# Performance work log

Hardware: AMD Instinct MI355X
Metric: run time of the kernel (lower is better)

## Reference

```python
import jax, jax.numpy as jnp
import numpy as np

EPS = 1e-5
NUM_GN_GROUPS = 32


def setup_inputs() -> dict:
    key = jax.random.key(0)
    k1, k2, k3 = jax.random.split(key, 3)
    B, C, N, G = 2, 256, 4096, 8
    c = C // G
    return {
        "points": jax.random.normal(k1, (B, C, N), dtype=jnp.float32),
        "conv_w": jax.random.normal(k2, (G, c, c), dtype=jnp.float32) / np.sqrt(c),
        "conv_b": jax.random.normal(k3, (C,), dtype=jnp.float32) * 0.02,
        "gn_w": jnp.ones((C,), dtype=jnp.float32),
        "gn_b": jnp.zeros((C,), dtype=jnp.float32),
    }


def reference(points, conv_w, conv_b, gn_w, gn_b):
    B, C, N = points.shape
    G = conv_w.shape[0]
    c = C // G  # channels per attention group
    identity = points

    # grouped 1x1 conv: per-group [c,c] matmul + bias
    x = points.reshape(B, G, c, N)
    x = jnp.einsum('gij,bgjn->bgin', conv_w, x) + conv_b.reshape(1, G, c, 1)

    # attention[b,g,n,m] = sum_i x[b,g,i,n] * x[b,g,i,m] / sqrt(c)
    scale = 1.0 / np.sqrt(c).astype(np.float32)
    attn = jnp.einsum('bgin,bgim->bgnm', x, x) * scale
    # softmax over dim=2 (the query/row N axis -- non-standard)
    attn = jax.nn.softmax(attn, axis=2)

    # ELU-gated second matmul: [B,G,c,N] @ [B,G,N,N] -> [B,G,c,N]
    x = jnp.einsum('bgcn,bgnm->bgcm', jax.nn.elu(x), attn)

    # channel shuffle: [B,G,c,N] -> [B,c,G,N] -> [B,C,N]
    x = x.transpose(0, 2, 1, 3).reshape(B, C, N)
    x = x + identity

    # GroupNorm(32 groups) over (channels-in-group, N)
    xg = x.reshape(B, NUM_GN_GROUPS, C // NUM_GN_GROUPS, N)
    mean = xg.mean(axis=(2, 3), keepdims=True)
    var = xg.var(axis=(2, 3), keepdims=True)
    xg = (xg - mean) * jax.lax.rsqrt(var + EPS)
    x = xg.reshape(B, C, N)
    return x * gn_w.reshape(1, C, 1) + gn_b.reshape(1, C, 1)
```

## Files before the change

### kernel.cpp

```cpp
#include <hip/hip_runtime.h>

typedef __attribute__((ext_vector_type(8))) short bf16x8;
typedef __attribute__((ext_vector_type(4))) short bf16x4;
typedef __attribute__((ext_vector_type(4))) float f32x4;

#if __has_builtin(__builtin_amdgcn_exp2f)
#define EXP2(x) __builtin_amdgcn_exp2f(x)
#else
#define EXP2(x) exp2f(x)
#endif

__device__ __forceinline__ unsigned short f2bf(float f) {
    union { float f; unsigned int u; } v; v.f = f;
    unsigned int r = v.u + 0x7fffu + ((v.u >> 16) & 1u);
    return (unsigned short)(r >> 16);
}

__device__ __forceinline__ float asf(unsigned int u) {
    union { unsigned int u; float f; } v; v.u = u; return v.f;
}

#define QK_PRESCALE 0.50500983f

__global__ __launch_bounds__(256) void conv_kernel(
    const float* __restrict__ points, const float* __restrict__ conv_w,
    const float* __restrict__ conv_b,
    unsigned short* __restrict__ xqT, unsigned short* __restrict__ xv)
{
    __shared__ float w[1024];
    const int h  = blockIdx.x >> 4;
    const int nc = blockIdx.x & 15;
    const int g  = h & 7;
    const int tid = threadIdx.x;
    const float* wg = conv_w + g * 1024;
    for (int k = tid; k < 1024; k += 256) w[k] = wg[k];
    __syncthreads();
    const int n = nc * 256 + tid;
    const float* p = points + (size_t)h * 32 * 4096 + n;
    float pv[32];
#pragma unroll
    for (int j = 0; j < 32; ++j) pv[j] = p[(size_t)j * 4096];
    float out[32];
#pragma unroll
    for (int i = 0; i < 32; ++i) {
        float acc = conv_b[g * 32 + i];
#pragma unroll
        for (int j = 0; j < 32; ++j) acc += w[i * 32 + j] * pv[j];
        out[i] = acc;
    }
    unsigned short tq[32];
#pragma unroll
    for (int i = 0; i < 32; ++i) tq[i] = f2bf(out[i] * QK_PRESCALE);
    bf16x8* dst = (bf16x8*)(xqT + ((size_t)h * 4096 + n) * 32);
#pragma unroll
    for (int t = 0; t < 4; ++t) dst[t] = ((bf16x8*)tq)[t];
#pragma unroll
    for (int i = 0; i < 32; ++i) {
        float x = out[i];
        float e = x > 0.f ? x : (__expf(x) - 1.f);
        xv[((size_t)h * 32 + i) * 4096 + n] = f2bf(e);
    }
}

#define KSTR 40
#define VSTR 136
#define PSTR 72

__device__ __forceinline__ bf16x4 exp_pack(f32x4 sc, float& lsum) {
    union { float f; unsigned int u; } e0, e1, e2, e3;
    e0.f = EXP2(sc[0]); e1.f = EXP2(sc[1]); e2.f = EXP2(sc[2]); e3.f = EXP2(sc[3]);
    unsigned int t0 = e0.u & 0xffff0000u, t1 = e1.u & 0xffff0000u;
    unsigned int t2 = e2.u & 0xffff0000u, t3 = e3.u & 0xffff0000u;
    lsum += (asf(t0) + asf(t1)) + (asf(t2) + asf(t3));
    union { unsigned int d[2]; bf16x4 v; } pk;
    pk.d[0] = (t0 >> 16) | t1;
    pk.d[1] = (t2 >> 16) | t3;
    return pk.v;
}

__global__ __launch_bounds__(256) void attn_kernel(
    const unsigned short* __restrict__ xqT,
    const unsigned short* __restrict__ xv,
    const float* __restrict__ points,
    float* __restrict__ z)
{
    __shared__ unsigned short Kt[128 * KSTR];
    __shared__ unsigned short Vt[32 * VSTR];
    __shared__ unsigned short Pl[4][16 * PSTR];

    const int h  = blockIdx.y;
    const int b = h >> 3, g = h & 7;
    const int tid = threadIdx.x;
    const int wv = tid >> 6, lane = tid & 63;
    const int quad = lane >> 4, l15 = lane & 15;

    const int m = blockIdx.x * 64 + wv * 16 + l15;

    const unsigned short* kbase = xqT + (size_t)h * 4096 * 32;
    const unsigned short* vbase = xv  + (size_t)h * 32 * 4096;

    const bf16x8 qfrag = *(const bf16x8*)(kbase + (size_t)m * 32 + quad * 8);

    f32x4 acc0 = {0.f, 0.f, 0.f, 0.f};
    f32x4 acc1 = {0.f, 0.f, 0.f, 0.f};
    float lsum = 0.f;

    const int kr = tid >> 2, kc = (tid & 3) * 8;
    const int vi = tid >> 3, vn = (tid & 7) * 8;

    unsigned short* pw = &Pl[wv][0];

    const unsigned short* kptrA = kbase + (size_t)kr * 32 + kc;
    const unsigned short* kptrB = kbase + (size_t)(64 + kr) * 32 + kc;
    const unsigned short* vptr  = vbase + (size_t)vi * 4096 + vn;
    bf16x8 ka = *(const bf16x8*)kptrA;
    bf16x8 kb = *(const bf16x8*)kptrB;
    bf16x8 va = *(const bf16x8*)vptr;
    bf16x8 vb = *(const bf16x8*)(vptr + 64);

    for (int n0 = 0; n0 < 4096; n0 += 128) {
        __syncthreads();
        *(bf16x8*)(Kt + kr * KSTR + kc)        = ka;
        *(bf16x8*)(Kt + (kr + 64) * KSTR + kc) = kb;
        *(bf16x8*)(Vt + vi * VSTR + vn)        = va;
        *(bf16x8*)(Vt + vi * VSTR + vn + 64)   = vb;
        __syncthreads();

        if (n0 + 128 < 4096) {
            kptrA += 128 * 32; kptrB += 128 * 32; vptr += 128;
            ka = *(const bf16x8*)kptrA;
            kb = *(const bf16x8*)kptrB;
            va = *(const bf16x8*)vptr;
            vb = *(const bf16x8*)(vptr + 64);
        }

#pragma unroll
        for (int sub = 0; sub < 2; ++sub) {
#pragma unroll
            for (int s = 0; s < 4; ++s) {
                bf16x8 kf = *(const bf16x8*)(
                    Kt + (sub * 64 + s * 16 + l15) * KSTR + quad * 8);
                f32x4 sc = __builtin_amdgcn_mfma_f32_16x16x32_bf16(
                    kf, qfrag, (f32x4){0.f, 0.f, 0.f, 0.f}, 0, 0, 0);
                bf16x4 pk = exp_pack(sc, lsum);
                *(bf16x4*)(pw + l15 * PSTR + s * 16 + quad * 4) = pk;
            }
#pragma unroll
            for (int ng = 0; ng < 2; ++ng) {
                bf16x8 pf = *(const bf16x8*)(pw + l15 * PSTR + ng * 32 + quad * 8);
                const int col = sub * 64 + ng * 32 + quad * 8;
                bf16x8 v0 = *(const bf16x8*)(Vt + l15 * VSTR + col);
                bf16x8 v1 = *(const bf16x8*)(Vt + (16 + l15) * VSTR + col);
                acc0 = __builtin_amdgcn_mfma_f32_16x16x32_bf16(v0, pf, acc0, 0, 0, 0);
                acc1 = __builtin_amdgcn_mfma_f32_16x16x32_bf16(v1, pf, acc1, 0, 0, 0);
            }
        }
    }

    lsum += __shfl_xor(lsum, 16, 64);
    lsum += __shfl_xor(lsum, 32, 64);
    const float inv = 1.f / lsum;

    const float* pb = points + (size_t)b * 256 * 4096;
    float* zb = z + (size_t)b * 256 * 4096;
#pragma unroll
    for (int half = 0; half < 2; ++half) {
        f32x4 a = half ? acc1 : acc0;
#pragma unroll
        for (int r = 0; r < 4; ++r) {
            int i = half * 16 + quad * 4 + r;
            size_t off = (size_t)(i * 8 + g) * 4096 + m;
            zb[off] = a[r] * inv + pb[off];
        }
    }
}

__global__ __launch_bounds__(256) void gn_stats(const float* __restrict__ z,
                                                float* __restrict__ stats)
{
    const int blk = blockIdx.x;
    const int tid = threadIdx.x;
    const float4* p = (const float4*)(z + (size_t)blk * 32768);
    float s = 0.f, ss = 0.f;
    for (int k = tid; k < 8192; k += 256) {
        float4 v = p[k];
        s  += v.x + v.y + v.z + v.w;
        ss += v.x * v.x + v.y * v.y + v.z * v.z + v.w * v.w;
    }
#pragma unroll
    for (int off = 32; off > 0; off >>= 1) {
        s  += __shfl_down(s, off, 64);
        ss += __shfl_down(ss, off, 64);
    }
    __shared__ float red[8];
    const int w = tid >> 6;
    if ((tid & 63) == 0) { red[w * 2] = s; red[w * 2 + 1] = ss; }
    __syncthreads();
    if (tid == 0) {
        s  = red[0] + red[2] + red[4] + red[6];
        ss = red[1] + red[3] + red[5] + red[7];
        float mean = s * (1.f / 32768.f);
        float var  = ss * (1.f / 32768.f) - mean * mean;
        stats[blk * 2]     = mean;
        stats[blk * 2 + 1] = rsqrtf(var + 1e-5f);
    }
}

__global__ __launch_bounds__(256) void gn_apply(float* __restrict__ z,
                                                const float* __restrict__ stats,
                                                const float* __restrict__ gw,
                                                const float* __restrict__ gb)
{
    const int idx = blockIdx.x * 256 + threadIdx.x;
    float4* p = (float4*)z;
    float4 v = p[idx];
    const int chg = idx >> 10;
    const int blk = chg >> 3;
    const int ch  = chg & 255;
    const float mean = stats[blk * 2], rstd = stats[blk * 2 + 1];
    const float w  = gw[ch] * rstd;
    const float bb = gb[ch] - mean * w;
    v.x = v.x * w + bb; v.y = v.y * w + bb;
    v.z = v.z * w + bb; v.w = v.w * w + bb;
    p[idx] = v;
}

extern "C" void kernel_launch(void* const* d_in, const int* in_sizes, int n_in,
                              void* d_out, int out_size, void* d_ws, size_t ws_size,
                              hipStream_t stream)
{
    const float* points = (const float*)d_in[0];
    const float* conv_w = (const float*)d_in[1];
    const float* conv_b = (const float*)d_in[2];
    const float* gn_w   = (const float*)d_in[3];
    const float* gn_b   = (const float*)d_in[4];
    float* out = (float*)d_out;
    char* ws = (char*)d_ws;
    unsigned short* xqT = (unsigned short*)ws;
    unsigned short* xv  = (unsigned short*)(ws + (size_t)4 * 1024 * 1024);
    float* stats = (float*)(ws + (size_t)8 * 1024 * 1024);

    conv_kernel<<<256, 256, 0, stream>>>(points, conv_w, conv_b, xqT, xv);
    attn_kernel<<<dim3(64, 16), 256, 0, stream>>>(xqT, xv, points, out);
    gn_stats<<<64, 256, 0, stream>>>(out, stats);
    gn_apply<<<2048, 256, 0, stream>>>(out, stats, gn_w, gn_b);
}
```

Baseline: 171.8 us.

## Split GN stats across more blocks, vectorize conv weight reads, use packed bf16 convert

GroupNorm statistics now run on 256 blocks that each reduce a quarter of a group and write partial sums. gn_apply combines the four partials per group and computes mean and rstd inline. The conv inner loop reads weights from shared memory as float4. The softmax exp packing uses the hardware packed bf16 convert (round-to-nearest) instead of truncation when that builtin exists, which slightly changes numerics and sums unrounded exps into lsum. The main cost targeted is the underparallelised 64-block stats pass.

```diff
diff --git a/kernel.cpp b/kernel.cpp
--- a/kernel.cpp
+++ b/kernel.cpp
@@ -44,8 +44,13 @@
 #pragma unroll
     for (int i = 0; i < 32; ++i) {
         float acc = conv_b[g * 32 + i];
-#pragma unroll
-        for (int j = 0; j < 32; ++j) acc += w[i * 32 + j] * pv[j];
+        const float4* w4 = (const float4*)(w + i * 32);
+#pragma unroll
+        for (int j4 = 0; j4 < 8; ++j4) {
+            float4 ww = w4[j4];
+            acc += ww.x * pv[j4 * 4]     + ww.y * pv[j4 * 4 + 1]
+                 + ww.z * pv[j4 * 4 + 2] + ww.w * pv[j4 * 4 + 3];
+        }
         out[i] = acc;
     }
     unsigned short tq[32];
@@ -66,6 +71,18 @@
 #define VSTR 136
 #define PSTR 72
 
+#if __has_builtin(__builtin_amdgcn_cvt_pk_bf16_f32)
+typedef __attribute__((ext_vector_type(2))) __bf16 bf16x2v;
+__device__ __forceinline__ bf16x4 exp_pack(f32x4 sc, float& lsum) {
+    float e0 = EXP2(sc[0]), e1 = EXP2(sc[1]);
+    float e2 = EXP2(sc[2]), e3 = EXP2(sc[3]);
+    lsum += (e0 + e1) + (e2 + e3);
+    union { bf16x2v v[2]; bf16x4 s; } u;
+    u.v[0] = __builtin_amdgcn_cvt_pk_bf16_f32(e0, e1);
+    u.v[1] = __builtin_amdgcn_cvt_pk_bf16_f32(e2, e3);
+    return u.s;
+}
+#else
 __device__ __forceinline__ bf16x4 exp_pack(f32x4 sc, float& lsum) {
     union { float f; unsigned int u; } e0, e1, e2, e3;
     e0.f = EXP2(sc[0]); e1.f = EXP2(sc[1]); e2.f = EXP2(sc[2]); e3.f = EXP2(sc[3]);
@@ -77,6 +94,7 @@
     pk.d[1] = (t2 >> 16) | t3;
     return pk.v;
 }
+#endif
 
 __global__ __launch_bounds__(256) void attn_kernel(
     const unsigned short* __restrict__ xqT,
@@ -176,13 +194,13 @@
 }
 
 __global__ __launch_bounds__(256) void gn_stats(const float* __restrict__ z,
-                                                float* __restrict__ stats)
+                                                float* __restrict__ pstats)
 {
     const int blk = blockIdx.x;
     const int tid = threadIdx.x;
-    const float4* p = (const float4*)(z + (size_t)blk * 32768);
+    const float4* p = (const float4*)(z + (size_t)blk * 8192);
     float s = 0.f, ss = 0.f;
-    for (int k = tid; k < 8192; k += 256) {
+    for (int k = tid; k < 2048; k += 256) {
         float4 v = p[k];
         s  += v.x + v.y + v.z + v.w;
         ss += v.x * v.x + v.y * v.y + v.z * v.z + v.w * v.w;
@@ -199,15 +217,13 @@
     if (tid == 0) {
         s  = red[0] + red[2] + red[4] + red[6];
         ss = red[1] + red[3] + red[5] + red[7];
-        float mean = s * (1.f / 32768.f);
-        float var  = ss * (1.f / 32768.f) - mean * mean;
-        stats[blk * 2]     = mean;
-        stats[blk * 2 + 1] = rsqrtf(var + 1e-5f);
+        pstats[blk * 2]     = s;
+        pstats[blk * 2 + 1] = ss;
     }
 }
 
 __global__ __launch_bounds__(256) void gn_apply(float* __restrict__ z,
-                                                const float* __restrict__ stats,
+                                                const float* __restrict__ pstats,
                                                 const float* __restrict__ gw,
                                                 const float* __restrict__ gb)
 {
@@ -215,9 +231,15 @@
     float4* p = (float4*)z;
     float4 v = p[idx];
     const int chg = idx >> 10;
-    const int blk = chg >> 3;
+    const int grp = chg >> 3;
     const int ch  = chg & 255;
-    const float mean = stats[blk * 2], rstd = stats[blk * 2 + 1];
+    const float4 s4  = *(const float4*)(pstats + grp * 8);
+    const float4 s4b = *(const float4*)(pstats + grp * 8 + 4);
+    const float s  = s4.x + s4.z + s4b.x + s4b.z;
+    const float ss = s4.y + s4.w + s4b.y + s4b.w;
+    const float mean = s * (1.f / 32768.f);
+    const float var  = ss * (1.f / 32768.f) - mean * mean;
+    const float rstd = rsqrtf(var + 1e-5f);
     const float w  = gw[ch] * rstd;
     const float bb = gb[ch] - mean * w;
     v.x = v.x * w + bb; v.y = v.y * w + bb;
@@ -238,10 +260,10 @@
     char* ws = (char*)d_ws;
     unsigned short* xqT = (unsigned short*)ws;
     unsigned short* xv  = (unsigned short*)(ws + (size_t)4 * 1024 * 1024);
-    float* stats = (float*)(ws + (size_t)8 * 1024 * 1024);
+    float* pstats = (float*)(ws + (size_t)8 * 1024 * 1024);
 
     conv_kernel<<<256, 256, 0, stream>>>(points, conv_w, conv_b, xqT, xv);
     attn_kernel<<<dim3(64, 16), 256, 0, stream>>>(xqT, xv, points, out);
-    gn_stats<<<64, 256, 0, stream>>>(out, stats);
-    gn_apply<<<2048, 256, 0, stream>>>(out, stats, gn_w, gn_b);
-}
+    gn_stats<<<256, 256, 0, stream>>>(out, pstats);
+    gn_apply<<<2048, 256, 0, stream>>>(out, pstats, gn_w, gn_b);
+}
```

Result: faster. 161.1 us (-6.3%).
